# Optimization experiments

Hardware: AMD Instinct MI355X
Metric: run time of the kernel (lower is better)

Reference implementation:

```python
import jax, jax.numpy as jnp
import numpy as np

B, L, F, H, O = 128, 2048, 128, 256, 128
NT = 5  # tickersteps


def setup_inputs() -> dict:
    key = jax.random.key(0)
    ks = jax.random.split(key, 10)
    x = jax.random.normal(ks[0], (B, L, F), dtype=jnp.float32)
    true_seq_lens = jax.random.randint(ks[1], (B,), 1, L + 1)
    s = 0.05
    W = jax.random.normal(ks[2], (F, 3 * H), dtype=jnp.float32) * s   # fwd weights [ci|ig|og]
    R = jax.random.normal(ks[3], (H, 3 * H), dtype=jnp.float32) * s   # recurrent weights [ci|ig|og]
    # biases: b_ci=0, b_ig ~ N(-5,1), b_og=0  (forget gate has no weights/bias -> fg = 1)
    b_ig = jax.random.normal(ks[4], (H,), dtype=jnp.float32) - 5.0
    b = jnp.concatenate([jnp.zeros(H, jnp.float32), b_ig, jnp.zeros(H, jnp.float32)])
    b_ticker = jax.random.normal(ks[5], (3 * H,), dtype=jnp.float32) * s  # tickerstep biases
    Wp = jax.random.normal(ks[6], (H, H), dtype=jnp.float32) * s
    bp = jnp.zeros((H,), jnp.float32)
    Wo = jax.random.normal(ks[7], (O, H), dtype=jnp.float32) * s
    bo = jnp.zeros((O,), jnp.float32)
    return {"x": x, "true_seq_lens": true_seq_lens, "W": W, "R": R, "b": b,
            "b_ticker": b_ticker, "Wp": Wp, "bp": bp, "Wo": Wo, "bo": bo}


def _lstm_final_h(x, true_seq_lens, W, R, b, b_ticker):
    Bv, Lv, _ = x.shape
    Hv = R.shape[0]
    T = Lv + NT
    xp = jnp.pad(x, ((0, 0), (0, NT), (0, 0)))            # zero input during tickersteps
    xs = jnp.swapaxes(xp, 0, 1)                            # [T, B, F]
    ts = jnp.arange(T)
    lens = true_seq_lens.astype(jnp.int32)

    def step(carry, inp):
        h, c = carry
        x_t, t = inp
        in_seq = t < lens                                  # [B]
        in_tick = (t >= lens) & (t < lens + NT)
        active = in_seq | in_tick
        x_t = jnp.where(in_seq[:, None], x_t, 0.0)
        pre = x_t @ W + h @ R + b + jnp.where(in_tick[:, None], b_ticker, 0.0)  # [B, 3H]
        ci = jnp.tanh(pre[:, :Hv])
        ig = jax.nn.sigmoid(pre[:, Hv:2 * Hv])
        og = jax.nn.sigmoid(pre[:, 2 * Hv:])
        c_new = c + ci * ig                                # forget gate disabled -> fg = 1
        h_new = jnp.tanh(c_new) * og
        m = active[:, None]
        return (jnp.where(m, h_new, h), jnp.where(m, c_new, c)), None

    h0 = jnp.zeros((Bv, Hv), x.dtype)
    c0 = jnp.zeros((Bv, Hv), x.dtype)
    (h, _), _ = jax.lax.scan(step, (h0, c0), (xs, ts))
    return h


def reference(x, true_seq_lens, W, R, b, b_ticker, Wp, bp, Wo, bo):
    h = _lstm_final_h(x, true_seq_lens, W, R, b, b_ticker)   # [B, H] final state after tickersteps
    h = h @ Wp.T + bp                                        # pre_fc_out
    return h @ Wo.T + bo                                     # fc_out
```

## Files before the change

kernel.cpp:

```cpp
#include <hip/hip_runtime.h>

#define BB    128
#define LL    2048
#define FF    128
#define HH    256
#define OO    128
#define NTICK 5
#define GC    16
#define NCG   8
#define CH    4
#define DRING 128
#define NPS   8
#define NPL   16
#define MAXT  (LL + NTICK)
#define MAXCH ((MAXT + CH - 1) / CH)
#define RDY8  0x0101010101010101ULL

typedef __attribute__((ext_vector_type(8))) _Float16 half8;
typedef __attribute__((ext_vector_type(4))) float f32x4;

union U64H8 { unsigned long long u[2]; _Float16 h[8]; };
union U64H4 { unsigned long long u; _Float16 h[4]; };

__device__ __forceinline__ float fast_rcp(float x) { return __builtin_amdgcn_rcpf(x); }

__device__ __forceinline__ unsigned long long sysload_u64(const unsigned long long* p) {
  return __hip_atomic_load(p, __ATOMIC_RELAXED, __HIP_MEMORY_SCOPE_SYSTEM);
}
__device__ __forceinline__ void sysstore_u64(unsigned long long* p, unsigned long long v) {
  __hip_atomic_store(p, v, __ATOMIC_RELAXED, __HIP_MEMORY_SCOPE_SYSTEM);
}
__device__ __forceinline__ int sysload_i32(const int* p) {
  return __hip_atomic_load(p, __ATOMIC_RELAXED, __HIP_MEMORY_SCOPE_SYSTEM);
}
__device__ __forceinline__ void sysstore_i32(int* p, int v) {
  __hip_atomic_store(p, v, __ATOMIC_RELAXED, __HIP_MEMORY_SCOPE_SYSTEM);
}
__device__ __forceinline__ void sysstore_u8(unsigned char* p, unsigned char v) {
  __hip_atomic_store(p, v, __ATOMIC_RELAXED, __HIP_MEMORY_SCOPE_SYSTEM);
}

extern "C" __global__ __launch_bounds__(512, 1)
void lstm_all(const float* __restrict__ x, const int* __restrict__ lens,
              const float* __restrict__ W, const float* __restrict__ R,
              const float* __restrict__ bvec, const float* __restrict__ btk,
              unsigned long long* ring, unsigned char* readyb,
              int* prog, float* __restrict__ h_final)
{
  const int tid  = threadIdx.x;
  const int lane = tid & 63;
  const int wv   = tid >> 6;
  const int quad = lane >> 4;
  const int nl   = lane & 15;
  const int bx   = blockIdx.x;

  __shared__ int lens_s[BB];
  if (tid < BB) lens_s[tid] = lens[tid];
  __syncthreads();

  if (bx < NCG) {
    const int cg = bx, cbase = cg * GC;
    __shared__ float    pre_s[GC][772];
    __shared__ float    c_s[GC][260];
    __shared__ _Float16 h_s[GC][264];

    for (int i = tid; i < GC * 772; i += 512) ((float*)pre_s)[i] = 0.f;
    for (int i = tid; i < GC * 260; i += 512) ((float*)c_s)[i] = 0.f;
    for (int i = tid; i < GC * 264; i += 512) ((_Float16*)h_s)[i] = (_Float16)0.f;

    int mxl = 0;
    #pragma unroll
    for (int i = 0; i < GC; i++) mxl = max(mxl, lens_s[cbase + i]);
    const int Tg = mxl + NTICK;

    half8 rfr[6][8];
    const int colw = wv * 96;
    #pragma unroll
    for (int tile = 0; tile < 6; tile++) {
      const int col = colw + tile * 16 + nl;
      #pragma unroll
      for (int kc = 0; kc < 8; kc++) {
        const int k0 = kc * 32 + quad * 8;
        half8 v;
        #pragma unroll
        for (int j = 0; j < 8; j++) v[j] = (_Float16)R[(k0 + j) * (3 * HH) + col];
        rfr[tile][kc] = v;
      }
    }

    const int m  = tid >> 5;
    const int hj = (tid & 31) * 8;
    const int lenm = lens_s[cbase + m];

    const unsigned long long* rb = (const unsigned long long*)readyb;

    while (sysload_u64(rb + 0) != RDY8) {}
    asm volatile("" ::: "memory");
    unsigned long long xw[6];
    {
      const unsigned long long* rp = ring + ((((long)0 * BB + cbase + m) * 768 + hj) >> 2);
      xw[0] = sysload_u64(rp);       xw[1] = sysload_u64(rp + 1);
      xw[2] = sysload_u64(rp + 64);  xw[3] = sysload_u64(rp + 65);
      xw[4] = sysload_u64(rp + 128); xw[5] = sysload_u64(rp + 129);
    }
    unsigned long long rvn = sysload_u64(rb + 1);
    int cur_chunk = 0;
    __syncthreads();

    for (int t = 0; t < Tg; ++t) {
      if (t > 0) {
        f32x4 acc[6];
        #pragma unroll
        for (int i = 0; i < 6; i++) acc[i] = (f32x4){0.f, 0.f, 0.f, 0.f};
        const _Float16* hrow = &h_s[nl][0];
        #pragma unroll
        for (int kc = 0; kc < 8; kc++) {
          const half8 a = *(const half8*)(hrow + kc * 32 + quad * 8);
          #pragma unroll
          for (int tile = 0; tile < 6; tile++)
            acc[tile] = __builtin_amdgcn_mfma_f32_16x16x32_f16(rfr[tile][kc], a, acc[tile], 0, 0, 0);
        }
        #pragma unroll
        for (int tile = 0; tile < 6; tile++)
          *(f32x4*)(&pre_s[nl][colw + tile * 16 + quad * 4]) = acc[tile];
      }
      __syncthreads();

      if (t < lenm + NTICK) {
        U64H8 uc, ui, uo;
        uc.u[0] = xw[0]; uc.u[1] = xw[1];
        ui.u[0] = xw[2]; ui.u[1] = xw[3];
        uo.u[0] = xw[4]; uo.u[1] = xw[5];
        const float* pr = &pre_s[m][0];
        float pci[8], pig[8], pog[8], cc[8], hh[8];
        *(float4*)(pci)     = *(const float4*)(pr + hj);
        *(float4*)(pci + 4) = *(const float4*)(pr + hj + 4);
        *(float4*)(pig)     = *(const float4*)(pr + 256 + hj);
        *(float4*)(pig + 4) = *(const float4*)(pr + 256 + hj + 4);
        *(float4*)(pog)     = *(const float4*)(pr + 512 + hj);
        *(float4*)(pog + 4) = *(const float4*)(pr + 512 + hj + 4);
        *(float4*)(cc)      = *(const float4*)(&c_s[m][hj]);
        *(float4*)(cc + 4)  = *(const float4*)(&c_s[m][hj + 4]);
        #pragma unroll
        for (int d = 0; d < 8; d++) {
          const float pc = pci[d] + (float)uc.h[d];
          const float pi = pig[d] + (float)ui.h[d];
          const float po = pog[d] + (float)uo.h[d];
          const float ea = __expf(2.f * __builtin_fminf(pc, 15.f));
          const float eb = __expf(-pi);
          const float cn = cc[d] + (ea - 1.f) * fast_rcp((ea + 1.f) * (1.f + eb));
          const float ec = __expf(2.f * __builtin_fminf(cn, 15.f));
          const float ed = __expf(-po);
          hh[d] = (ec - 1.f) * fast_rcp((ec + 1.f) * (1.f + ed));
          cc[d] = cn;
        }
        *(float4*)(&c_s[m][hj])     = *(float4*)(cc);
        *(float4*)(&c_s[m][hj + 4]) = *(float4*)(cc + 4);
        _Float16 hp8[8];
        #pragma unroll
        for (int d = 0; d < 8; d++) hp8[d] = (_Float16)hh[d];
        *(half8*)(&h_s[m][hj]) = *(half8*)hp8;
        if (t == lenm + NTICK - 1) {
          float* hf = h_final + (cbase + m) * HH + hj;
          *(float4*)(hf)     = *(float4*)(hh);
          *(float4*)(hf + 4) = *(float4*)(hh + 4);
        }
      }

      if (t + 1 < Tg) {
        const int nc = (t + 1) >> 2;
        if (nc != cur_chunk) {
          while (rvn != RDY8) rvn = sysload_u64(rb + nc);
          cur_chunk = nc;
          rvn = (nc + 1 < MAXCH) ? sysload_u64(rb + nc + 1) : RDY8;
        }
        asm volatile("" ::: "memory");
        const int slot = (t + 1) & (DRING - 1);
        const unsigned long long* rp = ring + ((((long)slot * BB + cbase + m) * 768 + hj) >> 2);
        xw[0] = sysload_u64(rp);       xw[1] = sysload_u64(rp + 1);
        xw[2] = sysload_u64(rp + 64);  xw[3] = sysload_u64(rp + 65);
        xw[4] = sysload_u64(rp + 128); xw[5] = sysload_u64(rp + 129);
      }
      __syncthreads();
      if (tid == 0) sysstore_i32(prog + cg, t);
    }
    if (tid == 0) sysstore_i32(prog + cg, 1 << 20);

  } else {
    const int pid = bx - NCG;
    const int s   = pid & 7;
    const int pl  = pid >> 3;

    int mxall = 0;
    #pragma unroll 8
    for (int i = 0; i < BB; i++) mxall = max(mxall, lens_s[i]);
    const int Tall = mxall + NTICK;
    const int nch  = (Tall + CH - 1) / CH;

    half8 wfr[4];
    float bias4[4], tick4[4];
    int col0w = 0;
    if (wv < 6) {
      col0w = s * 96 + wv * 16;
      #pragma unroll
      for (int kc = 0; kc < 4; kc++) {
        const int k0 = kc * 32 + quad * 8;
        half8 v;
        #pragma unroll
        for (int j = 0; j < 8; j++) v[j] = (_Float16)W[(k0 + j) * (3 * HH) + col0w + nl];
        wfr[kc] = v;
      }
      *(float4*)bias4 = *(const float4*)(bvec + col0w + quad * 4);
      *(float4*)tick4 = *(const float4*)(btk  + col0w + quad * 4);
    }

    for (int c = pl; c < nch; c += NPL) {
      if (c * CH >= DRING) {
        if (tid == 0) {
          const int need = c * CH + CH - DRING;
          for (;;) {
            int mn = 0x7fffffff;
            #pragma unroll
            for (int g = 0; g < NCG; g++) mn = min(mn, sysload_i32(prog + g));
            if (mn >= need) break;
          }
        }
        __syncthreads();
      }
      if (wv < 6) {
        for (int tt = 0; tt < CH; tt++) {
          const int t = c * CH + tt;
          const int slot = t & (DRING - 1);
          #pragma unroll 2
          for (int bt = 0; bt < 8; bt++) {
            const int b = bt * 16 + nl;
            const int lenb = lens_s[b];
            f32x4 acc = {0.f, 0.f, 0.f, 0.f};
            if (t < LL) {
              const float* xp = x + ((long)b * LL + t) * FF + quad * 8;
              #pragma unroll
              for (int kc = 0; kc < 4; kc++) {
                const float4 u0 = *(const float4*)(xp + kc * 32);
                const float4 u1 = *(const float4*)(xp + kc * 32 + 4);
                half8 a;
                a[0] = (_Float16)u0.x; a[1] = (_Float16)u0.y;
                a[2] = (_Float16)u0.z; a[3] = (_Float16)u0.w;
                a[4] = (_Float16)u1.x; a[5] = (_Float16)u1.y;
                a[6] = (_Float16)u1.z; a[7] = (_Float16)u1.w;
                acc = __builtin_amdgcn_mfma_f32_16x16x32_f16(wfr[kc], a, acc, 0, 0, 0);
              }
            }
            U64H4 pk;
            const bool in_x  = (t < lenb);
            const bool in_tk = (t >= lenb) && (t < lenb + NTICK);
            #pragma unroll
            for (int r = 0; r < 4; r++) {
              float v = bias4[r];
              if (in_x)  v += acc[r];
              if (in_tk) v += tick4[r];
              pk.h[r] = (_Float16)v;
            }
            sysstore_u64(ring + ((((long)slot * BB + b) * 768 + col0w + quad * 4) >> 2), pk.u);
          }
        }
      }
      __syncthreads();
      if (tid == 0) sysstore_u8(readyb + c * 8 + s, (unsigned char)1);
    }
  }
}

extern "C" __global__ void proj_hp(const float* __restrict__ h,
                                   const float* __restrict__ Wp,
                                   const float* __restrict__ bp,
                                   float* __restrict__ hp)
{
  const int bb = blockIdx.x;
  const int j  = threadIdx.x;
  const float4* hv = (const float4*)(h + bb * HH);
  const float4* wr = (const float4*)(Wp + j * HH);
  float s = 0.f;
  for (int k = 0; k < HH / 4; k++) {
    const float4 a = hv[k], w = wr[k];
    s += a.x * w.x + a.y * w.y + a.z * w.z + a.w * w.w;
  }
  hp[bb * HH + j] = s + bp[j];
}

extern "C" __global__ void proj_out(const float* __restrict__ hp,
                                    const float* __restrict__ Wo,
                                    const float* __restrict__ bo,
                                    float* __restrict__ out)
{
  const int bb = blockIdx.x;
  const int o  = threadIdx.x;
  const float4* hv = (const float4*)(hp + bb * HH);
  const float4* wr = (const float4*)(Wo + o * HH);
  float s = 0.f;
  for (int k = 0; k < HH / 4; k++) {
    const float4 a = hv[k], w = wr[k];
    s += a.x * w.x + a.y * w.y + a.z * w.z + a.w * w.w;
  }
  out[bb * OO + o] = s + bo[o];
}

extern "C" void kernel_launch(void* const* d_in, const int* in_sizes, int n_in,
                              void* d_out, int out_size, void* d_ws, size_t ws_size,
                              hipStream_t stream)
{
  const float* x    = (const float*)d_in[0];
  const int*   ln   = (const int*)  d_in[1];
  const float* W    = (const float*)d_in[2];
  const float* R    = (const float*)d_in[3];
  const float* bvec = (const float*)d_in[4];
  const float* btk  = (const float*)d_in[5];
  const float* Wp   = (const float*)d_in[6];
  const float* bp   = (const float*)d_in[7];
  const float* Wo   = (const float*)d_in[8];
  const float* bo   = (const float*)d_in[9];
  float* out = (float*)d_out;

  char* ws = (char*)d_ws;
  int*                prog    = (int*)ws;
  unsigned char*      readyb  = (unsigned char*)(ws + 64);
  float*              h_final = (float*)(ws + 8192);
  float*              hp      = (float*)(ws + 8192 + 131072);
  unsigned long long* ring    = (unsigned long long*)(ws + (1 << 20));

  hipLaunchKernelGGL(lstm_all, dim3(NCG + NPS * NPL), dim3(512), 0, stream,
                     x, ln, W, R, bvec, btk, ring, readyb, prog, h_final);
  hipLaunchKernelGGL(proj_hp,  dim3(BB), dim3(HH), 0, stream, h_final, Wp, bp, hp);
  hipLaunchKernelGGL(proj_out, dim3(BB), dim3(OO), 0, stream, hp, Wo, bo, out);
}
```

Baseline: 6.061 ms.

## Keep LSTM gate math in MFMA registers with double-buffered h

Reassigns recurrent-weight columns so each wave's MFMA output tiles hold matching ci/ig/og columns. The gate nonlinearity can then run straight on the accumulator registers, with the cell state kept in registers. This removes the pre-activation and cell-state round trips through shared memory and one of the two block barriers per timestep. h is double-buffered in LDS so a single barrier per step is enough, at the cost of more register pressure and an inline-asm waitcnt plus raw s_barrier.

```diff
diff --git a/kernel.cpp b/kernel.cpp
--- a/kernel.cpp
+++ b/kernel.cpp
@@ -19,7 +19,6 @@
 typedef __attribute__((ext_vector_type(8))) _Float16 half8;
 typedef __attribute__((ext_vector_type(4))) float f32x4;
 
-union U64H8 { unsigned long long u[2]; _Float16 h[8]; };
 union U64H4 { unsigned long long u; _Float16 h[4]; };
 
 __device__ __forceinline__ float fast_rcp(float x) { return __builtin_amdgcn_rcpf(x); }
@@ -60,24 +59,18 @@
 
   if (bx < NCG) {
     const int cg = bx, cbase = cg * GC;
-    __shared__ float    pre_s[GC][772];
-    __shared__ float    c_s[GC][260];
-    __shared__ _Float16 h_s[GC][264];
-
-    for (int i = tid; i < GC * 772; i += 512) ((float*)pre_s)[i] = 0.f;
-    for (int i = tid; i < GC * 260; i += 512) ((float*)c_s)[i] = 0.f;
-    for (int i = tid; i < GC * 264; i += 512) ((_Float16*)h_s)[i] = (_Float16)0.f;
+    __shared__ _Float16 h_s[2][GC][264];
 
     int mxl = 0;
     #pragma unroll
     for (int i = 0; i < GC; i++) mxl = max(mxl, lens_s[cbase + i]);
-    const int Tg = mxl + NTICK;
+    const int Tg   = mxl + NTICK;
+    const int lenn = lens_s[cbase + nl];
 
     half8 rfr[6][8];
-    const int colw = wv * 96;
     #pragma unroll
     for (int tile = 0; tile < 6; tile++) {
-      const int col = colw + tile * 16 + nl;
+      const int col = (tile >> 1) * 256 + wv * 32 + (tile & 1) * 16 + nl;
       #pragma unroll
       for (int kc = 0; kc < 8; kc++) {
         const int k0 = kc * 32 + quad * 8;
@@ -88,83 +81,81 @@
       }
     }
 
-    const int m  = tid >> 5;
-    const int hj = (tid & 31) * 8;
-    const int lenm = lens_s[cbase + m];
+    float cst[8], hreg[8];
+    #pragma unroll
+    for (int i = 0; i < 8; i++) { cst[i] = 0.f; hreg[i] = 0.f; }
+
+    const int o0 = wv * 32 + quad * 4;
 
     const unsigned long long* rb = (const unsigned long long*)readyb;
-
-    while (sysload_u64(rb + 0) != RDY8) {}
+    while (sysload_u64(rb) != RDY8) {}
     asm volatile("" ::: "memory");
     unsigned long long xw[6];
     {
-      const unsigned long long* rp = ring + ((((long)0 * BB + cbase + m) * 768 + hj) >> 2);
-      xw[0] = sysload_u64(rp);       xw[1] = sysload_u64(rp + 1);
-      xw[2] = sysload_u64(rp + 64);  xw[3] = sysload_u64(rp + 65);
-      xw[4] = sysload_u64(rp + 128); xw[5] = sysload_u64(rp + 129);
+      const unsigned long long* rp = ring + ((((long)cbase + nl) * 768) >> 2);
+      xw[0] = sysload_u64(rp + ((o0      ) >> 2));
+      xw[1] = sysload_u64(rp + ((o0 +  16) >> 2));
+      xw[2] = sysload_u64(rp + ((o0 + 256) >> 2));
+      xw[3] = sysload_u64(rp + ((o0 + 272) >> 2));
+      xw[4] = sysload_u64(rp + ((o0 + 512) >> 2));
+      xw[5] = sysload_u64(rp + ((o0 + 528) >> 2));
     }
     unsigned long long rvn = sysload_u64(rb + 1);
     int cur_chunk = 0;
     __syncthreads();
 
     for (int t = 0; t < Tg; ++t) {
+      f32x4 acc[6];
+      #pragma unroll
+      for (int i = 0; i < 6; i++) acc[i] = (f32x4){0.f, 0.f, 0.f, 0.f};
+
       if (t > 0) {
-        f32x4 acc[6];
-        #pragma unroll
-        for (int i = 0; i < 6; i++) acc[i] = (f32x4){0.f, 0.f, 0.f, 0.f};
-        const _Float16* hrow = &h_s[nl][0];
+        const _Float16* hb = &h_s[(t - 1) & 1][nl][quad * 8];
         #pragma unroll
         for (int kc = 0; kc < 8; kc++) {
-          const half8 a = *(const half8*)(hrow + kc * 32 + quad * 8);
+          const half8 a = *(const half8*)(hb + kc * 32);
           #pragma unroll
           for (int tile = 0; tile < 6; tile++)
             acc[tile] = __builtin_amdgcn_mfma_f32_16x16x32_f16(rfr[tile][kc], a, acc[tile], 0, 0, 0);
         }
-        #pragma unroll
-        for (int tile = 0; tile < 6; tile++)
-          *(f32x4*)(&pre_s[nl][colw + tile * 16 + quad * 4]) = acc[tile];
-      }
-      __syncthreads();
-
-      if (t < lenm + NTICK) {
-        U64H8 uc, ui, uo;
-        uc.u[0] = xw[0]; uc.u[1] = xw[1];
-        ui.u[0] = xw[2]; ui.u[1] = xw[3];
-        uo.u[0] = xw[4]; uo.u[1] = xw[5];
-        const float* pr = &pre_s[m][0];
-        float pci[8], pig[8], pog[8], cc[8], hh[8];
-        *(float4*)(pci)     = *(const float4*)(pr + hj);
-        *(float4*)(pci + 4) = *(const float4*)(pr + hj + 4);
-        *(float4*)(pig)     = *(const float4*)(pr + 256 + hj);
-        *(float4*)(pig + 4) = *(const float4*)(pr + 256 + hj + 4);
-        *(float4*)(pog)     = *(const float4*)(pr + 512 + hj);
-        *(float4*)(pog + 4) = *(const float4*)(pr + 512 + hj + 4);
-        *(float4*)(cc)      = *(const float4*)(&c_s[m][hj]);
-        *(float4*)(cc + 4)  = *(const float4*)(&c_s[m][hj + 4]);
-        #pragma unroll
-        for (int d = 0; d < 8; d++) {
-          const float pc = pci[d] + (float)uc.h[d];
-          const float pi = pig[d] + (float)ui.h[d];
-          const float po = pog[d] + (float)uo.h[d];
-          const float ea = __expf(2.f * __builtin_fminf(pc, 15.f));
-          const float eb = __expf(-pi);
-          const float cn = cc[d] + (ea - 1.f) * fast_rcp((ea + 1.f) * (1.f + eb));
-          const float ec = __expf(2.f * __builtin_fminf(cn, 15.f));
-          const float ed = __expf(-po);
-          hh[d] = (ec - 1.f) * fast_rcp((ec + 1.f) * (1.f + ed));
-          cc[d] = cn;
-        }
-        *(float4*)(&c_s[m][hj])     = *(float4*)(cc);
-        *(float4*)(&c_s[m][hj + 4]) = *(float4*)(cc + 4);
-        _Float16 hp8[8];
-        #pragma unroll
-        for (int d = 0; d < 8; d++) hp8[d] = (_Float16)hh[d];
-        *(half8*)(&h_s[m][hj]) = *(half8*)hp8;
-        if (t == lenm + NTICK - 1) {
-          float* hf = h_final + (cbase + m) * HH + hj;
-          *(float4*)(hf)     = *(float4*)(hh);
-          *(float4*)(hf + 4) = *(float4*)(hh + 4);
-        }
+      }
+
+      if (t < lenn + NTICK) {
+        #pragma unroll
+        for (int tt = 0; tt < 2; tt++) {
+          U64H4 xc, xi, xo2;
+          xc.u = xw[tt]; xi.u = xw[2 + tt]; xo2.u = xw[4 + tt];
+          #pragma unroll
+          for (int r = 0; r < 4; r++) {
+            const float pc = acc[tt][r]     + (float)xc.h[r];
+            const float pi = acc[2 + tt][r] + (float)xi.h[r];
+            const float po = acc[4 + tt][r] + (float)xo2.h[r];
+            const float ea = __expf(2.f * __builtin_fminf(pc, 15.f));
+            const float eb = __expf(-pi);
+            const float cn = cst[tt * 4 + r] + (ea - 1.f) * fast_rcp((ea + 1.f) * (1.f + eb));
+            const float ec = __expf(2.f * __builtin_fminf(cn, 15.f));
+            const float ed = __expf(-po);
+            hreg[tt * 4 + r] = (ec - 1.f) * fast_rcp((ec + 1.f) * (1.f + ed));
+            cst[tt * 4 + r] = cn;
+          }
+        }
+        if (t == lenn + NTICK - 1) {
+          float* hf = h_final + (cbase + nl) * HH + wv * 32 + quad * 4;
+          *(float4*)hf        = make_float4(hreg[0], hreg[1], hreg[2], hreg[3]);
+          *(float4*)(hf + 16) = make_float4(hreg[4], hreg[5], hreg[6], hreg[7]);
+        }
+      }
+
+      {
+        U64H4 p0, p1;
+        #pragma unroll
+        for (int r = 0; r < 4; r++) {
+          p0.h[r] = (_Float16)hreg[r];
+          p1.h[r] = (_Float16)hreg[4 + r];
+        }
+        _Float16* hw = &h_s[t & 1][nl][o0];
+        *(unsigned long long*)hw        = p0.u;
+        *(unsigned long long*)(hw + 16) = p1.u;
       }
 
       if (t + 1 < Tg) {
@@ -173,16 +164,21 @@
           while (rvn != RDY8) rvn = sysload_u64(rb + nc);
           cur_chunk = nc;
           rvn = (nc + 1 < MAXCH) ? sysload_u64(rb + nc + 1) : RDY8;
-        }
-        asm volatile("" ::: "memory");
+          asm volatile("" ::: "memory");
+        }
         const int slot = (t + 1) & (DRING - 1);
-        const unsigned long long* rp = ring + ((((long)slot * BB + cbase + m) * 768 + hj) >> 2);
-        xw[0] = sysload_u64(rp);       xw[1] = sysload_u64(rp + 1);
-        xw[2] = sysload_u64(rp + 64);  xw[3] = sysload_u64(rp + 65);
-        xw[4] = sysload_u64(rp + 128); xw[5] = sysload_u64(rp + 129);
-      }
-      __syncthreads();
+        const unsigned long long* rp = ring + ((((long)slot * BB + cbase + nl) * 768) >> 2);
+        xw[0] = sysload_u64(rp + ((o0      ) >> 2));
+        xw[1] = sysload_u64(rp + ((o0 +  16) >> 2));
+        xw[2] = sysload_u64(rp + ((o0 + 256) >> 2));
+        xw[3] = sysload_u64(rp + ((o0 + 272) >> 2));
+        xw[4] = sysload_u64(rp + ((o0 + 512) >> 2));
+        xw[5] = sysload_u64(rp + ((o0 + 528) >> 2));
+      }
       if (tid == 0) sysstore_i32(prog + cg, t);
+
+      asm volatile("s_waitcnt lgkmcnt(0)" ::: "memory");
+      __builtin_amdgcn_s_barrier();
     }
     if (tid == 0) sysstore_i32(prog + cg, 1 << 20);
 
```

Result: slower. 7.800 ms (+28.7%).
